# Kernel tuning notes

Measured on AMD Instinct MI355X. Metric: run time of the kernel, lower is better.

## Reference

```python
import jax, jax.numpy as jnp
import numpy as np

NUM_EXPERTS = 8
TOP_K = 2
AUX_COEF = 0.01
B, S, D, H = 4, 2048, 1024, 684


def setup_inputs() -> dict:
    key = jax.random.key(0)
    ks = jax.random.split(key, 5)
    scale_d = 1.0 / np.sqrt(D)
    scale_h = 1.0 / np.sqrt(H)
    return {
        "x": jax.random.normal(ks[0], (B, S, D), dtype=jnp.float32),
        "router_w": jax.random.normal(ks[1], (NUM_EXPERTS, D), dtype=jnp.float32) * scale_d,
        "w1": jax.random.normal(ks[2], (NUM_EXPERTS, H, D), dtype=jnp.float32) * scale_d,
        "w2": jax.random.normal(ks[3], (NUM_EXPERTS, D, H), dtype=jnp.float32) * scale_h,
        "w3": jax.random.normal(ks[4], (NUM_EXPERTS, H, D), dtype=jnp.float32) * scale_d,
    }


def reference(x, router_w, w1, w2, w3):
    b, s, d = x.shape
    xf = x.reshape(-1, d)                                   # [T, d]
    probs = jax.nn.softmax(xf @ router_w.T, axis=-1)        # [T, E]
    topk_probs, topk_idx = jax.lax.top_k(probs, TOP_K)      # [T, k]

    # aux load-balancing loss (uses top-1 assignment density)
    density = jnp.mean(jax.nn.one_hot(topk_idx[:, 0], NUM_EXPERTS, dtype=xf.dtype), axis=0)
    aux_loss = AUX_COEF * jnp.sum(density * probs.mean(axis=0)) * NUM_EXPERTS

    # per-token per-expert combine weight (sums probs if an expert repeats across slots)
    combine = jnp.sum(jax.nn.one_hot(topk_idx, NUM_EXPERTS, dtype=xf.dtype)
                      * topk_probs[..., None], axis=1)      # [T, E]

    out = jnp.zeros_like(xf)
    for e in range(NUM_EXPERTS):  # fixed small expert loop
        h = jax.nn.silu(xf @ w1[e].T) * (xf @ w3[e].T)      # [T, H] SwiGLU
        out = out + combine[:, e:e + 1] * (h @ w2[e].T)     # weighted scatter-combine
    return out.reshape(b, s, d), aux_loss
```

## Files before the change

### kernel.cpp

```cpp
#include <hip/hip_runtime.h>
#include <hip/hip_bf16.h>

#define T_TOK 8192
#define DMODEL 1024
#define HDIM 684
#define HPAD 704
#define NEXP 8

typedef short  bf16x8  __attribute__((ext_vector_type(8)));
typedef float  f32x4   __attribute__((ext_vector_type(4)));

__device__ inline unsigned short f2bu(float f) {
    __hip_bfloat16 h = __float2bfloat16(f);
    return *reinterpret_cast<unsigned short*>(&h);
}

typedef const __attribute__((address_space(1))) unsigned int* gas_p;
typedef __attribute__((address_space(3))) unsigned int* las_p;
__device__ inline void ld_lds16(const unsigned short* g, unsigned short* l) {
    __builtin_amdgcn_global_load_lds((gas_p)g, (las_p)l, 16, 0, 0);
}

#define POS_OFF    74252800ull
#define PAIRS_OFF  74318336ull
#define WS_NEED   141427200ull

__global__ __launch_bounds__(256) void cvt_all(
    const float* __restrict__ w1, const float* __restrict__ w3, const float* __restrict__ w2,
    unsigned short* __restrict__ w1b, unsigned short* __restrict__ w3b,
    unsigned short* __restrict__ w2b, int n4, int n2)
{
    int i = blockIdx.x * 256 + threadIdx.x;
    if (i < 2 * n4) {
        const float* src; unsigned short* dst; int j;
        if (i < n4) { src = w1; dst = w1b; j = i; }
        else        { src = w3; dst = w3b; j = i - n4; }
        float4 v = ((const float4*)src)[j];
        ((ushort4*)dst)[j] = make_ushort4(f2bu(v.x), f2bu(v.y), f2bu(v.z), f2bu(v.w));
        return;
    }
    int j = i - 2 * n4;
    if (j >= n2) return;
    int row = j / 176;
    int col = (j - row * 176) * 4;
    ushort4 o = make_ushort4(0, 0, 0, 0);
    if (col < HDIM) {
        float4 v = *(const float4*)(w2 + (size_t)row * HDIM + col);
        o = make_ushort4(f2bu(v.x), f2bu(v.y), f2bu(v.z), f2bu(v.w));
    }
    *(ushort4*)(w2b + (size_t)row * HPAD + col) = o;
}

__global__ __launch_bounds__(256) void moe_router(
    const float* __restrict__ x, const float* __restrict__ rw,
    unsigned short* __restrict__ xb,
    float* __restrict__ blk_psum, int* __restrict__ blk_t1, int* __restrict__ blk_pc,
    int* __restrict__ topk_idx, float* __restrict__ topk_p)
{
    __shared__ float sp[4][NEXP];
    __shared__ int   si1[4], si2[4];

    int lane = threadIdx.x & 63;
    int w    = threadIdx.x >> 6;
    int t    = blockIdx.x * 4 + w;
    const float* xr = x + (size_t)t * DMODEL;
    unsigned short* xbr = xb + (size_t)t * DMODEL;

    float acc[NEXP];
#pragma unroll
    for (int e = 0; e < NEXP; ++e) acc[e] = 0.f;
#pragma unroll
    for (int j = 0; j < DMODEL / 64; ++j) {
        float xv = xr[j * 64 + lane];
        xbr[j * 64 + lane] = f2bu(xv);
#pragma unroll
        for (int e = 0; e < NEXP; ++e)
            acc[e] += xv * rw[e * DMODEL + j * 64 + lane];
    }
#pragma unroll
    for (int off = 32; off > 0; off >>= 1) {
#pragma unroll
        for (int e = 0; e < NEXP; ++e)
            acc[e] += __shfl_xor(acc[e], off, 64);
    }
    if (lane == 0) {
        float m = acc[0];
#pragma unroll
        for (int e = 1; e < NEXP; ++e) m = fmaxf(m, acc[e]);
        float p[NEXP]; float s = 0.f;
#pragma unroll
        for (int e = 0; e < NEXP; ++e) { p[e] = expf(acc[e] - m); s += p[e]; }
        float inv = 1.f / s;
#pragma unroll
        for (int e = 0; e < NEXP; ++e) p[e] *= inv;
        int i1 = 0;
#pragma unroll
        for (int e = 1; e < NEXP; ++e) if (p[e] > p[i1]) i1 = e;
        int i2 = (i1 == 0) ? 1 : 0;
#pragma unroll
        for (int e = 0; e < NEXP; ++e) if (e != i1 && p[e] > p[i2]) i2 = e;

        topk_idx[t * 2 + 0] = i1;  topk_idx[t * 2 + 1] = i2;
        topk_p[t * 2 + 0] = p[i1]; topk_p[t * 2 + 1] = p[i2];
#pragma unroll
        for (int e = 0; e < NEXP; ++e) sp[w][e] = p[e];
        si1[w] = i1; si2[w] = i2;
    }
    __syncthreads();
    if (threadIdx.x < NEXP) {
        int e = threadIdx.x;
        float ps = sp[0][e] + sp[1][e] + sp[2][e] + sp[3][e];
        int t1 = (si1[0] == e) + (si1[1] == e) + (si1[2] == e) + (si1[3] == e);
        int pc = t1 + (si2[0] == e) + (si2[1] == e) + (si2[2] == e) + (si2[3] == e);
        blk_psum[blockIdx.x * NEXP + e] = ps;
        blk_t1[blockIdx.x * NEXP + e]  = t1;
        blk_pc[blockIdx.x * NEXP + e]  = pc;
    }
}

__global__ __launch_bounds__(256) void moe_scan(
    const float* __restrict__ blk_psum, const int* __restrict__ blk_t1,
    const int* __restrict__ blk_pc,
    int* pair_count, int* offsets, int* cursor, float* aux_out)
{
    __shared__ float wp[4][NEXP];
    __shared__ int   wt[4][NEXP], wc[4][NEXP];
    __shared__ float tp[NEXP];
    __shared__ int   tt1[NEXP], tpc[NEXP];

    int tid = threadIdx.x;
    int lane = tid & 63, w = tid >> 6;
    float lp[NEXP]; int lt[NEXP], lc[NEXP];
#pragma unroll
    for (int e = 0; e < NEXP; ++e) { lp[e] = 0.f; lt[e] = 0; lc[e] = 0; }
    for (int b = tid; b < 2048; b += 256)
#pragma unroll
        for (int e = 0; e < NEXP; ++e) {
            lp[e] += blk_psum[b * NEXP + e];
            lt[e] += blk_t1[b * NEXP + e];
            lc[e] += blk_pc[b * NEXP + e];
        }
#pragma unroll
    for (int off = 32; off > 0; off >>= 1) {
#pragma unroll
        for (int e = 0; e < NEXP; ++e) {
            lp[e] += __shfl_xor(lp[e], off, 64);
            lt[e] += __shfl_xor(lt[e], off, 64);
            lc[e] += __shfl_xor(lc[e], off, 64);
        }
    }
    if (lane == 0) {
#pragma unroll
        for (int e = 0; e < NEXP; ++e) { wp[w][e] = lp[e]; wt[w][e] = lt[e]; wc[w][e] = lc[e]; }
    }
    __syncthreads();
    if (tid < NEXP) {
        int e = tid;
        float s = wp[0][e] + wp[1][e] + wp[2][e] + wp[3][e];
        int t1 = wt[0][e] + wt[1][e] + wt[2][e] + wt[3][e];
        int pc = wc[0][e] + wc[1][e] + wc[2][e] + wc[3][e];
        tp[e] = s; tt1[e] = t1; tpc[e] = pc;
        pair_count[e] = pc;
    }
    __syncthreads();
    if (tid == 0) {
        int run = 0;
        for (int e = 0; e < NEXP; ++e) { offsets[e] = run; cursor[e] = run; run += tpc[e]; }
        float s = 0.f;
        for (int e = 0; e < NEXP; ++e)
            s += ((float)tt1[e] / (float)T_TOK) * (tp[e] / (float)T_TOK);
        aux_out[0] = 0.01f * s * (float)NEXP;
    }
}

__global__ __launch_bounds__(256) void moe_scatter(
    const int* __restrict__ topk_idx, const float* __restrict__ topk_p,
    int* cursor, int* __restrict__ pair_token, float* __restrict__ pair_prob,
    int* __restrict__ pos)
{
    __shared__ int lcnt[NEXP], gbase[NEXP];
    int tid = threadIdx.x;
    if (tid < NEXP) lcnt[tid] = 0;
    __syncthreads();
    int t = blockIdx.x * 256 + tid;
    int e0 = topk_idx[t * 2 + 0], e1 = topk_idx[t * 2 + 1];
    int p0 = atomicAdd(&lcnt[e0], 1);
    int p1 = atomicAdd(&lcnt[e1], 1);
    __syncthreads();
    if (tid < NEXP) gbase[tid] = atomicAdd(&cursor[tid], lcnt[tid]);
    __syncthreads();
    int q0 = gbase[e0] + p0, q1 = gbase[e1] + p1;
    pair_token[q0] = t; pair_prob[q0] = topk_p[t * 2 + 0];
    pair_token[q1] = t; pair_prob[q1] = topk_p[t * 2 + 1];
    pos[t * 2 + 0] = q0; pos[t * 2 + 1] = q1;
}


__global__ __launch_bounds__(256, 2) void moe_ffn1(
    const unsigned short* __restrict__ xb, const unsigned short* __restrict__ w1b,
    const unsigned short* __restrict__ w3b,
    const int* __restrict__ pair_count, const int* __restrict__ offsets,
    const int* __restrict__ pair_token,
    unsigned short* __restrict__ h)
{
    int e   = blockIdx.z;
    int cnt = pair_count[e];
    int m0  = blockIdx.y * 128;
    if (m0 >= cnt) return;
    int base = offsets[e];
    int n0   = blockIdx.x * 128;

    __shared__ unsigned short aT[3 * 4096];
    __shared__ unsigned short b1T[3 * 4096];
    __shared__ unsigned short b3T[3 * 4096];

    int tid  = threadIdx.x;
    int lane = tid & 63, wave = tid >> 6;
    int wm = wave >> 1, wn = wave & 1;

    int srow = lane >> 2;
    int ksg  = (lane & 3) ^ ((lane >> 3) & 3);
    int ar0 = m0 + wave * 16 + srow;      if (ar0 >= cnt) ar0 = cnt - 1;
    int ar1 = m0 + 64 + wave * 16 + srow; if (ar1 >= cnt) ar1 = cnt - 1;
    const unsigned short* ap0 = xb + (size_t)pair_token[base + ar0] * DMODEL + ksg * 8;
    const unsigned short* ap1 = xb + (size_t)pair_token[base + ar1] * DMODEL + ksg * 8;
    int br0 = n0 + wave * 16 + srow;      if (br0 > HDIM - 1) br0 = HDIM - 1;
    int br1 = n0 + 64 + wave * 16 + srow; if (br1 > HDIM - 1) br1 = HDIM - 1;
    const unsigned short* b1p0 = w1b + ((size_t)e * HDIM + br0) * DMODEL + ksg * 8;
    const unsigned short* b1p1 = w1b + ((size_t)e * HDIM + br1) * DMODEL + ksg * 8;
    const unsigned short* b3p0 = w3b + ((size_t)e * HDIM + br0) * DMODEL + ksg * 8;
    const unsigned short* b3p1 = w3b + ((size_t)e * HDIM + br1) * DMODEL + ksg * 8;
    int wof0 = wave * 512, wof1 = 2048 + wave * 512;

#define STAGE_F1(bf, koff) do { \
    ld_lds16(ap0  + (koff), aT  + (bf) * 4096 + wof0); \
    ld_lds16(ap1  + (koff), aT  + (bf) * 4096 + wof1); \
    ld_lds16(b1p0 + (koff), b1T + (bf) * 4096 + wof0); \
    ld_lds16(b1p1 + (koff), b1T + (bf) * 4096 + wof1); \
    ld_lds16(b3p0 + (koff), b3T + (bf) * 4096 + wof0); \
    ld_lds16(b3p1 + (koff), b3T + (bf) * 4096 + wof1); \
  } while (0)

    f32x4 acc1[4][4], acc3[4][4];
#pragma unroll
    for (int i = 0; i < 4; ++i)
#pragma unroll
        for (int j = 0; j < 4; ++j) { acc1[i][j] = (f32x4)(0.f); acc3[i][j] = (f32x4)(0.f); }

    int fr  = lane & 15;
    int sz8 = ((lane >> 4) ^ ((fr >> 1) & 3)) * 8;

    STAGE_F1(0, 0);
    STAGE_F1(1, 32);

    const int NIT = DMODEL / 32;
    for (int it = 0; it < NIT; ++it) {
        int buf = it % 3;
        if (it + 1 < NIT) asm volatile("s_waitcnt vmcnt(6)" ::: "memory");
        else              asm volatile("s_waitcnt vmcnt(0)" ::: "memory");
        __builtin_amdgcn_s_barrier();
        asm volatile("" ::: "memory");
        if (it + 2 < NIT) STAGE_F1((it + 2) % 3, (it + 2) * 32);

        const unsigned short* cA  = aT  + buf * 4096;
        const unsigned short* cB1 = b1T + buf * 4096;
        const unsigned short* cB3 = b3T + buf * 4096;

        bf16x8 aF[4];
#pragma unroll
        for (int i = 0; i < 4; ++i)
            aF[i] = *(const bf16x8*)&cA[(wm * 64 + i * 16 + fr) * 32 + sz8];
        __builtin_amdgcn_s_setprio(1);
#pragma unroll
        for (int j = 0; j < 4; ++j) {
            int row = (wn * 64 + j * 16 + fr) * 32 + sz8;
            bf16x8 b1F = *(const bf16x8*)&cB1[row];
            bf16x8 b3F = *(const bf16x8*)&cB3[row];
#pragma unroll
            for (int i = 0; i < 4; ++i) {
                acc1[i][j] = __builtin_amdgcn_mfma_f32_16x16x32_bf16(aF[i], b1F, acc1[i][j], 0, 0, 0);
                acc3[i][j] = __builtin_amdgcn_mfma_f32_16x16x32_bf16(aF[i], b3F, acc3[i][j], 0, 0, 0);
            }
        }
        __builtin_amdgcn_s_setprio(0);
    }
#undef STAGE_F1

    int cbase = n0 + wn * 64 + fr;
    int rbase = m0 + wm * 64 + (lane >> 4) * 4;
#pragma unroll
    for (int i = 0; i < 4; ++i) {
#pragma unroll
        for (int r = 0; r < 4; ++r) {
            int gr = rbase + i * 16 + r;
            if (gr >= cnt) continue;
            unsigned short* hrow = h + (size_t)(base + gr) * HPAD;
#pragma unroll
            for (int j = 0; j < 4; ++j) {
                int col = cbase + j * 16;
                if (col >= HPAD) continue;
                float v1 = acc1[i][j][r];
                float hv = (col < HDIM) ? (v1 / (1.f + expf(-v1))) * acc3[i][j][r] : 0.f;
                hrow[col] = f2bu(hv);
            }
        }
    }
}

__global__ __launch_bounds__(256, 2) void moe_ffn2(
    const unsigned short* __restrict__ h, const unsigned short* __restrict__ w2b,
    const int* __restrict__ pair_count, const int* __restrict__ offsets,
    const int* __restrict__ pair_token, const float* __restrict__ pair_prob,
    float* __restrict__ pairs_out, float* __restrict__ out, int use_atomic)
{
    int e   = blockIdx.z;
    int cnt = pair_count[e];
    int m0  = blockIdx.y * 128;
    if (m0 >= cnt) return;
    int base = offsets[e];
    int n0   = blockIdx.x * 256;

    __shared__ unsigned short aT[3 * 4096];
    __shared__ unsigned short bT[3 * 8192];

    int tid  = threadIdx.x;
    int lane = tid & 63, wave = tid >> 6;
    int wm = wave >> 1, wn = wave & 1;

    int srow = lane >> 2;
    int ksg  = (lane & 3) ^ ((lane >> 3) & 3);
    int ar0 = m0 + wave * 16 + srow;      if (ar0 >= cnt) ar0 = cnt - 1;
    int ar1 = m0 + 64 + wave * 16 + srow; if (ar1 >= cnt) ar1 = cnt - 1;
    const unsigned short* ap0 = h + (size_t)(base + ar0) * HPAD + ksg * 8;
    const unsigned short* ap1 = h + (size_t)(base + ar1) * HPAD + ksg * 8;
    int brr = n0 + wave * 16 + srow;
    const unsigned short* bp0 = w2b + ((size_t)e * DMODEL + brr)       * HPAD + ksg * 8;
    const unsigned short* bp1 = w2b + ((size_t)e * DMODEL + brr + 64)  * HPAD + ksg * 8;
    const unsigned short* bp2 = w2b + ((size_t)e * DMODEL + brr + 128) * HPAD + ksg * 8;
    const unsigned short* bp3 = w2b + ((size_t)e * DMODEL + brr + 192) * HPAD + ksg * 8;
    int wof = wave * 512;

#define STAGE_F2(bf, koff) do { \
    ld_lds16(ap0 + (koff), aT + (bf) * 4096 + wof); \
    ld_lds16(ap1 + (koff), aT + (bf) * 4096 + wof + 2048); \
    ld_lds16(bp0 + (koff), bT + (bf) * 8192 + wof); \
    ld_lds16(bp1 + (koff), bT + (bf) * 8192 + wof + 2048); \
    ld_lds16(bp2 + (koff), bT + (bf) * 8192 + wof + 4096); \
    ld_lds16(bp3 + (koff), bT + (bf) * 8192 + wof + 6144); \
  } while (0)

    f32x4 acc[4][8];
#pragma unroll
    for (int i = 0; i < 4; ++i)
#pragma unroll
        for (int j = 0; j < 8; ++j) acc[i][j] = (f32x4)(0.f);

    int fr  = lane & 15;
    int sz8 = ((lane >> 4) ^ ((fr >> 1) & 3)) * 8;

    STAGE_F2(0, 0);
    STAGE_F2(1, 32);

    const int NIT = HPAD / 32;
    for (int it = 0; it < NIT; ++it) {
        int buf = it % 3;
        if (it + 1 < NIT) asm volatile("s_waitcnt vmcnt(6)" ::: "memory");
        else              asm volatile("s_waitcnt vmcnt(0)" ::: "memory");
        __builtin_amdgcn_s_barrier();
        asm volatile("" ::: "memory");
        if (it + 2 < NIT) STAGE_F2((it + 2) % 3, (it + 2) * 32);

        const unsigned short* cA = aT + buf * 4096;
        const unsigned short* cB = bT + buf * 8192;

        bf16x8 aF[4];
#pragma unroll
        for (int i = 0; i < 4; ++i)
            aF[i] = *(const bf16x8*)&cA[(wm * 64 + i * 16 + fr) * 32 + sz8];
        __builtin_amdgcn_s_setprio(1);
#pragma unroll
        for (int j = 0; j < 8; ++j) {
            bf16x8 bF = *(const bf16x8*)&cB[(wn * 128 + j * 16 + fr) * 32 + sz8];
#pragma unroll
            for (int i = 0; i < 4; ++i)
                acc[i][j] = __builtin_amdgcn_mfma_f32_16x16x32_bf16(aF[i], bF, acc[i][j], 0, 0, 0);
        }
        __builtin_amdgcn_s_setprio(0);
    }
#undef STAGE_F2

    int cbase = n0 + wn * 128 + fr;
    int rbase = m0 + wm * 64 + (lane >> 4) * 4;
#pragma unroll
    for (int i = 0; i < 4; ++i) {
#pragma unroll
        for (int r = 0; r < 4; ++r) {
            int gr = rbase + i * 16 + r;
            if (gr >= cnt) continue;
            int gp = base + gr;
            float pw = pair_prob[gp];
            if (!use_atomic) {
                float* prow = pairs_out + (size_t)gp * DMODEL;
#pragma unroll
                for (int j = 0; j < 8; ++j)
                    prow[cbase + j * 16] = pw * acc[i][j][r];
            } else {
                float* orow = out + (size_t)pair_token[gp] * DMODEL;
#pragma unroll
                for (int j = 0; j < 8; ++j)
                    atomicAdd(&orow[cbase + j * 16], pw * acc[i][j][r]);
            }
        }
    }
}

__global__ __launch_bounds__(256) void moe_combine(
    const float* __restrict__ pairs_out, const int* __restrict__ pos,
    float* __restrict__ out)
{
    int t = blockIdx.x;
    int c = threadIdx.x;
    int q0 = pos[t * 2 + 0], q1 = pos[t * 2 + 1];
    float4 a = ((const float4*)(pairs_out + (size_t)q0 * DMODEL))[c];
    float4 b = ((const float4*)(pairs_out + (size_t)q1 * DMODEL))[c];
    float4 o;
    o.x = a.x + b.x; o.y = a.y + b.y; o.z = a.z + b.z; o.w = a.w + b.w;
    ((float4*)(out + (size_t)t * DMODEL))[c] = o;
}

extern "C" void kernel_launch(void* const* d_in, const int* in_sizes, int n_in,
                              void* d_out, int out_size, void* d_ws, size_t ws_size,
                              hipStream_t stream)
{
    const float* x  = (const float*)d_in[0];
    const float* rw = (const float*)d_in[1];
    const float* w1 = (const float*)d_in[2];
    const float* w2 = (const float*)d_in[3];
    const float* w3 = (const float*)d_in[4];
    float* out = (float*)d_out;

    char* ws = (char*)d_ws;
    int*   pair_count = (int*)(ws + 0);
    int*   offsets    = (int*)(ws + 32);
    int*   cursor     = (int*)(ws + 64);
    float* blk_psum   = (float*)(ws + 256);
    int*   blk_t1     = (int*)(ws + 65792);
    int*   blk_pc     = (int*)(ws + 131328);
    int*   topk_idx   = (int*)(ws + 196864);
    float* topk_p     = (float*)(ws + 262400);
    int*   pair_token = (int*)(ws + 327936);
    float* pair_prob  = (float*)(ws + 393472);
    unsigned short* xb  = (unsigned short*)(ws + 459264);
    unsigned short* w1b = (unsigned short*)(ws + 17236480);
    unsigned short* w3b = (unsigned short*)(ws + 28443136);
    unsigned short* w2b = (unsigned short*)(ws + 39649792);
    unsigned short* hbuf= (unsigned short*)(ws + 51184128);
    int*   pos        = (int*)(ws + POS_OFF);
    float* pairs_out  = (float*)(ws + PAIRS_OFF);

    int two_pass = (ws_size >= WS_NEED) ? 1 : 0;
    if (!two_pass)
        hipMemsetAsync(d_out, 0, (size_t)out_size * sizeof(float), stream);

    int n4 = NEXP * HDIM * DMODEL / 4;
    int n2 = NEXP * DMODEL * (HPAD / 4);
    cvt_all<<<(2 * n4 + n2 + 255) / 256, 256, 0, stream>>>(w1, w3, w2, w1b, w3b, w2b, n4, n2);

    moe_router <<<T_TOK / 4, 256, 0, stream>>>(x, rw, xb, blk_psum, blk_t1, blk_pc, topk_idx, topk_p);
    moe_scan   <<<1, 256, 0, stream>>>(blk_psum, blk_t1, blk_pc, pair_count, offsets, cursor,
                                       out + (size_t)T_TOK * DMODEL);
    moe_scatter<<<T_TOK / 256, 256, 0, stream>>>(topk_idx, topk_p, cursor, pair_token, pair_prob, pos);

    moe_ffn1<<<dim3(6, 64, 8), 256, 0, stream>>>(xb, w1b, w3b, pair_count, offsets, pair_token, hbuf);
    moe_ffn2<<<dim3(4, 64, 8), 256, 0, stream>>>(hbuf, w2b, pair_count, offsets, pair_token, pair_prob,
                                                 pairs_out, out, two_pass ? 0 : 1);
    if (two_pass)
        moe_combine<<<T_TOK, 256, 0, stream>>>(pairs_out, pos, out);
}
```

Measured before the change: 320.0 us.

## Enlarge MoE FFN GEMM tiles to 512-thread blocks and vectorize router loads

Both expert GEMM kernels move to 512-thread blocks with 8 waves. ffn1 now covers 128x256 output tiles and ffn2 covers 256x256 tiles with a 4-deep LDS ring, and ffn2 prefetches three stages ahead. In both kernels the next-stage global-to-LDS copies are issued after the MFMA loop instead of before it. The goal is more data reuse per LDS byte loaded and fewer redundant weight and activation fetches. The router reads x and router weights as float4 to cut load instructions. The cost is much larger LDS footprints (about 120 KB and 128 KB), which likely limits each CU to one block and reduces latency hiding.

```diff
diff --git a/kernel.cpp b/kernel.cpp
--- a/kernel.cpp
+++ b/kernel.cpp
@@ -63,19 +63,21 @@
     int lane = threadIdx.x & 63;
     int w    = threadIdx.x >> 6;
     int t    = blockIdx.x * 4 + w;
-    const float* xr = x + (size_t)t * DMODEL;
-    unsigned short* xbr = xb + (size_t)t * DMODEL;
+    const float4* xr4 = (const float4*)(x + (size_t)t * DMODEL);
+    ushort4* xbr4 = (ushort4*)(xb + (size_t)t * DMODEL);
 
     float acc[NEXP];
 #pragma unroll
     for (int e = 0; e < NEXP; ++e) acc[e] = 0.f;
 #pragma unroll
-    for (int j = 0; j < DMODEL / 64; ++j) {
-        float xv = xr[j * 64 + lane];
-        xbr[j * 64 + lane] = f2bu(xv);
-#pragma unroll
-        for (int e = 0; e < NEXP; ++e)
-            acc[e] += xv * rw[e * DMODEL + j * 64 + lane];
+    for (int j = 0; j < DMODEL / 256; ++j) {
+        float4 xv = xr4[j * 64 + lane];
+        xbr4[j * 64 + lane] = make_ushort4(f2bu(xv.x), f2bu(xv.y), f2bu(xv.z), f2bu(xv.w));
+#pragma unroll
+        for (int e = 0; e < NEXP; ++e) {
+            float4 rv = ((const float4*)(rw + (size_t)e * DMODEL))[j * 64 + lane];
+            acc[e] += xv.x * rv.x + xv.y * rv.y + xv.z * rv.z + xv.w * rv.w;
+        }
     }
 #pragma unroll
     for (int off = 32; off > 0; off >>= 1) {
@@ -196,7 +198,7 @@
 }
 
 
-__global__ __launch_bounds__(256, 2) void moe_ffn1(
+__global__ __launch_bounds__(512, 2) void moe_ffn1(
     const unsigned short* __restrict__ xb, const unsigned short* __restrict__ w1b,
     const unsigned short* __restrict__ w3b,
     const int* __restrict__ pair_count, const int* __restrict__ offsets,
@@ -208,37 +210,33 @@
     int m0  = blockIdx.y * 128;
     if (m0 >= cnt) return;
     int base = offsets[e];
-    int n0   = blockIdx.x * 128;
-
-    __shared__ unsigned short aT[3 * 4096];
-    __shared__ unsigned short b1T[3 * 4096];
-    __shared__ unsigned short b3T[3 * 4096];
+    int n0   = blockIdx.x * 256;
+
+    __shared__ unsigned short aT [3 * 4096];
+    __shared__ unsigned short b1T[3 * 8192];
+    __shared__ unsigned short b3T[3 * 8192];
 
     int tid  = threadIdx.x;
     int lane = tid & 63, wave = tid >> 6;
-    int wm = wave >> 1, wn = wave & 1;
+    int wm = wave >> 2, wn = wave & 3;
 
     int srow = lane >> 2;
     int ksg  = (lane & 3) ^ ((lane >> 3) & 3);
-    int ar0 = m0 + wave * 16 + srow;      if (ar0 >= cnt) ar0 = cnt - 1;
-    int ar1 = m0 + 64 + wave * 16 + srow; if (ar1 >= cnt) ar1 = cnt - 1;
-    const unsigned short* ap0 = xb + (size_t)pair_token[base + ar0] * DMODEL + ksg * 8;
-    const unsigned short* ap1 = xb + (size_t)pair_token[base + ar1] * DMODEL + ksg * 8;
-    int br0 = n0 + wave * 16 + srow;      if (br0 > HDIM - 1) br0 = HDIM - 1;
-    int br1 = n0 + 64 + wave * 16 + srow; if (br1 > HDIM - 1) br1 = HDIM - 1;
+    int ar = m0 + wave * 16 + srow; if (ar >= cnt) ar = cnt - 1;
+    const unsigned short* ap = xb + (size_t)pair_token[base + ar] * DMODEL + ksg * 8;
+    int br0 = n0 + wave * 32 + srow;      if (br0 > HDIM - 1) br0 = HDIM - 1;
+    int br1 = n0 + wave * 32 + srow + 16; if (br1 > HDIM - 1) br1 = HDIM - 1;
     const unsigned short* b1p0 = w1b + ((size_t)e * HDIM + br0) * DMODEL + ksg * 8;
     const unsigned short* b1p1 = w1b + ((size_t)e * HDIM + br1) * DMODEL + ksg * 8;
     const unsigned short* b3p0 = w3b + ((size_t)e * HDIM + br0) * DMODEL + ksg * 8;
     const unsigned short* b3p1 = w3b + ((size_t)e * HDIM + br1) * DMODEL + ksg * 8;
-    int wof0 = wave * 512, wof1 = 2048 + wave * 512;
-
-#define STAGE_F1(bf, koff) do { \
-    ld_lds16(ap0  + (koff), aT  + (bf) * 4096 + wof0); \
-    ld_lds16(ap1  + (koff), aT  + (bf) * 4096 + wof1); \
-    ld_lds16(b1p0 + (koff), b1T + (bf) * 4096 + wof0); \
-    ld_lds16(b1p1 + (koff), b1T + (bf) * 4096 + wof1); \
-    ld_lds16(b3p0 + (koff), b3T + (bf) * 4096 + wof0); \
-    ld_lds16(b3p1 + (koff), b3T + (bf) * 4096 + wof1); \
+
+#define STAGE_F1(slot, koff) do { \
+    ld_lds16(ap   + (koff), aT  + (slot) * 4096 + wave * 512); \
+    ld_lds16(b1p0 + (koff), b1T + (slot) * 8192 + wave * 1024); \
+    ld_lds16(b1p1 + (koff), b1T + (slot) * 8192 + wave * 1024 + 512); \
+    ld_lds16(b3p0 + (koff), b3T + (slot) * 8192 + wave * 1024); \
+    ld_lds16(b3p1 + (koff), b3T + (slot) * 8192 + wave * 1024 + 512); \
   } while (0)
 
     f32x4 acc1[4][4], acc3[4][4];
@@ -255,16 +253,15 @@
 
     const int NIT = DMODEL / 32;
     for (int it = 0; it < NIT; ++it) {
-        int buf = it % 3;
-        if (it + 1 < NIT) asm volatile("s_waitcnt vmcnt(6)" ::: "memory");
+        int slot = it % 3;
+        if (it + 1 < NIT) asm volatile("s_waitcnt vmcnt(5)" ::: "memory");
         else              asm volatile("s_waitcnt vmcnt(0)" ::: "memory");
         __builtin_amdgcn_s_barrier();
         asm volatile("" ::: "memory");
-        if (it + 2 < NIT) STAGE_F1((it + 2) % 3, (it + 2) * 32);
-
-        const unsigned short* cA  = aT  + buf * 4096;
-        const unsigned short* cB1 = b1T + buf * 4096;
-        const unsigned short* cB3 = b3T + buf * 4096;
+
+        const unsigned short* cA  = aT  + slot * 4096;
+        const unsigned short* cB1 = b1T + slot * 8192;
+        const unsigned short* cB3 = b3T + slot * 8192;
 
         bf16x8 aF[4];
 #pragma unroll
@@ -283,6 +280,8 @@
             }
         }
         __builtin_amdgcn_s_setprio(0);
+
+        if (it + 2 < NIT) STAGE_F1((it + 2) % 3, (it + 2) * 32);
     }
 #undef STAGE_F1
 
@@ -307,7 +306,7 @@
     }
 }
 
-__global__ __launch_bounds__(256, 2) void moe_ffn2(
+__global__ __launch_bounds__(512, 2) void moe_ffn2(
     const unsigned short* __restrict__ h, const unsigned short* __restrict__ w2b,
     const int* __restrict__ pair_count, const int* __restrict__ offsets,
     const int* __restrict__ pair_token, const float* __restrict__ pair_prob,
@@ -315,84 +314,82 @@
 {
     int e   = blockIdx.z;
     int cnt = pair_count[e];
-    int m0  = blockIdx.y * 128;
+    int m0  = blockIdx.y * 256;
     if (m0 >= cnt) return;
     int base = offsets[e];
     int n0   = blockIdx.x * 256;
 
-    __shared__ unsigned short aT[3 * 4096];
-    __shared__ unsigned short bT[3 * 8192];
+    __shared__ unsigned short aT[4 * 8192];
+    __shared__ unsigned short bT[4 * 8192];
 
     int tid  = threadIdx.x;
     int lane = tid & 63, wave = tid >> 6;
-    int wm = wave >> 1, wn = wave & 1;
+    int wm = wave >> 2, wn = wave & 3;
 
     int srow = lane >> 2;
     int ksg  = (lane & 3) ^ ((lane >> 3) & 3);
-    int ar0 = m0 + wave * 16 + srow;      if (ar0 >= cnt) ar0 = cnt - 1;
-    int ar1 = m0 + 64 + wave * 16 + srow; if (ar1 >= cnt) ar1 = cnt - 1;
+    int ar0 = m0 + wave * 32 + srow;      if (ar0 >= cnt) ar0 = cnt - 1;
+    int ar1 = m0 + wave * 32 + srow + 16; if (ar1 >= cnt) ar1 = cnt - 1;
     const unsigned short* ap0 = h + (size_t)(base + ar0) * HPAD + ksg * 8;
     const unsigned short* ap1 = h + (size_t)(base + ar1) * HPAD + ksg * 8;
-    int brr = n0 + wave * 16 + srow;
-    const unsigned short* bp0 = w2b + ((size_t)e * DMODEL + brr)       * HPAD + ksg * 8;
-    const unsigned short* bp1 = w2b + ((size_t)e * DMODEL + brr + 64)  * HPAD + ksg * 8;
-    const unsigned short* bp2 = w2b + ((size_t)e * DMODEL + brr + 128) * HPAD + ksg * 8;
-    const unsigned short* bp3 = w2b + ((size_t)e * DMODEL + brr + 192) * HPAD + ksg * 8;
-    int wof = wave * 512;
-
-#define STAGE_F2(bf, koff) do { \
-    ld_lds16(ap0 + (koff), aT + (bf) * 4096 + wof); \
-    ld_lds16(ap1 + (koff), aT + (bf) * 4096 + wof + 2048); \
-    ld_lds16(bp0 + (koff), bT + (bf) * 8192 + wof); \
-    ld_lds16(bp1 + (koff), bT + (bf) * 8192 + wof + 2048); \
-    ld_lds16(bp2 + (koff), bT + (bf) * 8192 + wof + 4096); \
-    ld_lds16(bp3 + (koff), bT + (bf) * 8192 + wof + 6144); \
+    int brr = n0 + wave * 32 + srow;
+    const unsigned short* bp0 = w2b + ((size_t)e * DMODEL + brr)      * HPAD + ksg * 8;
+    const unsigned short* bp1 = w2b + ((size_t)e * DMODEL + brr + 16) * HPAD + ksg * 8;
+
+#define STAGE_F2(slot, koff) do { \
+    ld_lds16(ap0 + (koff), aT + (slot) * 8192 + wave * 1024); \
+    ld_lds16(ap1 + (koff), aT + (slot) * 8192 + wave * 1024 + 512); \
+    ld_lds16(bp0 + (koff), bT + (slot) * 8192 + wave * 1024); \
+    ld_lds16(bp1 + (koff), bT + (slot) * 8192 + wave * 1024 + 512); \
   } while (0)
 
-    f32x4 acc[4][8];
-#pragma unroll
-    for (int i = 0; i < 4; ++i)
-#pragma unroll
-        for (int j = 0; j < 8; ++j) acc[i][j] = (f32x4)(0.f);
+    f32x4 acc[8][4];
+#pragma unroll
+    for (int i = 0; i < 8; ++i)
+#pragma unroll
+        for (int j = 0; j < 4; ++j) acc[i][j] = (f32x4)(0.f);
 
     int fr  = lane & 15;
     int sz8 = ((lane >> 4) ^ ((fr >> 1) & 3)) * 8;
 
     STAGE_F2(0, 0);
     STAGE_F2(1, 32);
+    STAGE_F2(2, 64);
 
     const int NIT = HPAD / 32;
     for (int it = 0; it < NIT; ++it) {
-        int buf = it % 3;
-        if (it + 1 < NIT) asm volatile("s_waitcnt vmcnt(6)" ::: "memory");
-        else              asm volatile("s_waitcnt vmcnt(0)" ::: "memory");
+        int slot = it % 4;
+        if      (it < NIT - 2) asm volatile("s_waitcnt vmcnt(8)" ::: "memory");
+        else if (it == NIT - 2) asm volatile("s_waitcnt vmcnt(4)" ::: "memory");
+        else                    asm volatile("s_waitcnt vmcnt(0)" ::: "memory");
         __builtin_amdgcn_s_barrier();
         asm volatile("" ::: "memory");
-        if (it + 2 < NIT) STAGE_F2((it + 2) % 3, (it + 2) * 32);
-
-        const unsigned short* cA = aT + buf * 4096;
-        const unsigned short* cB = bT + buf * 8192;
-
-        bf16x8 aF[4];
-#pragma unroll
-        for (int i = 0; i < 4; ++i)
-            aF[i] = *(const bf16x8*)&cA[(wm * 64 + i * 16 + fr) * 32 + sz8];
+
+        const unsigned short* cA = aT + slot * 8192;
+        const unsigned short* cB = bT + slot * 8192;
+
+        bf16x8 aF[8];
+#pragma unroll
+        for (int i = 0; i < 8; ++i)
+            aF[i] = *(const bf16x8*)&cA[(wm * 128 + i * 16 + fr) * 32 + sz8];
         __builtin_amdgcn_s_setprio(1);
 #pragma unroll
-        for (int j = 0; j < 8; ++j) {
-            bf16x8 bF = *(const bf16x8*)&cB[(wn * 128 + j * 16 + fr) * 32 + sz8];
-#pragma unroll
-            for (int i = 0; i < 4; ++i)
+        for (int j = 0; j < 4; ++j) {
+            bf16x8 bF = *(const bf16x8*)&cB[(wn * 64 + j * 16 + fr) * 32 + sz8];
+#pragma unroll
+            for (int i = 0; i < 8; ++i)
                 acc[i][j] = __builtin_amdgcn_mfma_f32_16x16x32_bf16(aF[i], bF, acc[i][j], 0, 0, 0);
         }
         __builtin_amdgcn_s_setprio(0);
+
+        if (it + 3 < NIT) STAGE_F2((it + 3) % 4, (it + 3) * 32);
     }
 #undef STAGE_F2
 
-    int cbase = n0 + wn * 128 + fr;
-    int rbase = m0 + wm * 64 + (lane >> 4) * 4;
-#pragma unroll
-    for (int i = 0; i < 4; ++i) {
+    int cbase = n0 + wn * 64 + fr;
+    int rbase = m0 + wm * 128 + (lane >> 4) * 4;
+#pragma unroll
+    for (int i = 0; i < 8; ++i) {
 #pragma unroll
         for (int r = 0; r < 4; ++r) {
             int gr = rbase + i * 16 + r;
@@ -402,12 +399,12 @@
             if (!use_atomic) {
                 float* prow = pairs_out + (size_t)gp * DMODEL;
 #pragma unroll
-                for (int j = 0; j < 8; ++j)
+                for (int j = 0; j < 4; ++j)
                     prow[cbase + j * 16] = pw * acc[i][j][r];
             } else {
                 float* orow = out + (size_t)pair_token[gp] * DMODEL;
 #pragma unroll
-                for (int j = 0; j < 8; ++j)
+                for (int j = 0; j < 4; ++j)
                     atomicAdd(&orow[cbase + j * 16], pw * acc[i][j][r]);
             }
         }
@@ -471,8 +468,8 @@
                                        out + (size_t)T_TOK * DMODEL);
     moe_scatter<<<T_TOK / 256, 256, 0, stream>>>(topk_idx, topk_p, cursor, pair_token, pair_prob, pos);
 
-    moe_ffn1<<<dim3(6, 64, 8), 256, 0, stream>>>(xb, w1b, w3b, pair_count, offsets, pair_token, hbuf);
-    moe_ffn2<<<dim3(4, 64, 8), 256, 0, stream>>>(hbuf, w2b, pair_count, offsets, pair_token, pair_prob,
+    moe_ffn1<<<dim3(3, 128, 8), 512, 0, stream>>>(xb, w1b, w3b, pair_count, offsets, pair_token, hbuf);
+    moe_ffn2<<<dim3(4, 64, 8), 512, 0, stream>>>(hbuf, w2b, pair_count, offsets, pair_token, pair_prob,
                                                  pairs_out, out, two_pass ? 0 : 1);
     if (two_pass)
         moe_combine<<<T_TOK, 256, 0, stream>>>(pairs_out, pos, out);
```

Result: no change. 319.7 us (-0.1%).
